# Kernel optimization log

Hardware: AMD Instinct MI355X
Metric: run time of the kernel (lower is better)

The kernel has to match this reference:

```python
import jax, jax.numpy as jnp
import numpy as np

B, KLEN, QLEN = 16, 4096, 1
D_MODEL, HEADS, KERNELS = 1024, 8, 10
DIM = D_MODEL // HEADS  # 128
SCALE = 0.02


def setup_inputs() -> dict:
    key = jax.random.key(0)
    ks = jax.random.split(key, 12)
    return {
        "query": jax.random.normal(ks[0], (B, QLEN, D_MODEL), jnp.float32),
        "key_in": jax.random.normal(ks[1], (B, KLEN, D_MODEL), jnp.float32),
        "value": jax.random.normal(ks[2], (B, KLEN, D_MODEL), jnp.float32),
        "prev_align": jax.random.uniform(ks[3], (B, HEADS, KLEN), jnp.float32),
        # learned params
        "conv_w": jax.random.normal(ks[4], (KERNELS, HEADS, 3), jnp.float32) * SCALE,   # OIH, k=3
        "conv_b": jnp.zeros((KERNELS,), jnp.float32),
        "w_u": jax.random.normal(ks[5], (KERNELS, DIM), jnp.float32) * SCALE,
        "w_q": jax.random.normal(ks[6], (D_MODEL, HEADS * DIM), jnp.float32) * SCALE,
        "w_v": jax.random.normal(ks[7], (D_MODEL, HEADS * DIM), jnp.float32) * SCALE,
        "bias": jax.random.uniform(ks[8], (DIM,), jnp.float32, minval=-0.1, maxval=0.1),
        "score_w": jax.random.normal(ks[9], (DIM,), jnp.float32) * SCALE,
        "score_b": jnp.zeros((), jnp.float32),
    }


def reference(query, key_in, value, prev_align, conv_w, conv_b, w_u, w_q, w_v, bias, score_w, score_b):
    b, k_len = key_in.shape[0], key_in.shape[1]
    # location features: conv1d over k_len with heads as channels -> [B, KERNELS, k_len]
    loc = jax.lax.conv_general_dilated(
        prev_align, conv_w, window_strides=(1,), padding=[(1, 1)],
        dimension_numbers=("NCH", "OIH", "NCH")) + conv_b[None, :, None]
    loc_energy = jnp.tanh(jnp.einsum("bck,cd->bkd", loc, w_u))  # [B, k_len, DIM]
    # projections split into heads
    q = jnp.einsum("bqf,fe->bqe", query, w_q).reshape(b, QLEN, HEADS, DIM).transpose(0, 2, 1, 3)   # [B,H,1,DIM]
    k = jnp.einsum("bkf,fe->bke", key_in, w_v).reshape(b, k_len, HEADS, DIM).transpose(0, 2, 1, 3)  # [B,H,K,DIM]
    v = value.reshape(b, k_len, HEADS, DIM).transpose(0, 2, 1, 3)                                   # [B,H,K,DIM]
    # additive energy (q_len==1 broadcasts over keys)
    e = jnp.tanh(k + q + loc_energy[:, None] + bias)            # [B,H,K,DIM]
    score = jnp.einsum("bhkd,d->bhk", e, score_w) + score_b    # [B,H,K]
    align = jax.nn.softmax(score, axis=-1)
    context = jnp.einsum("bhk,bhkd->bhd", align, v).reshape(b * HEADS, DIM)
    return context, align
```

## Files before the change

kernel.cpp:

```cpp
#include <hip/hip_runtime.h>
#include <hip/hip_bf16.h>
#include <cstdint>

typedef __attribute__((ext_vector_type(8))) short bf16x8;
typedef __attribute__((ext_vector_type(4))) float f32x4;
typedef __attribute__((ext_vector_type(8))) unsigned short u16x8;
typedef __attribute__((ext_vector_type(4))) unsigned int u32x4;

__device__ __forceinline__ unsigned short f2bf(float f) {
    unsigned int u = __float_as_uint(f);
    unsigned int r = (u + 0x7fffu + ((u >> 16) & 1u)) >> 16;
    return (unsigned short)r;
}

__device__ __forceinline__ float tanh_fast(float x) {
    return 1.0f - 2.0f / (__expf(2.0f * x) + 1.0f);
}

#define GLDS(SRC, DST) __builtin_amdgcn_global_load_lds(                         \
        (const __attribute__((address_space(1))) void*)(SRC),                    \
        (__attribute__((address_space(3))) void*)(DST), 16, 0, 0)

__global__ __launch_bounds__(256) void prep_kernel(
        const float* __restrict__ wv, unsigned short* __restrict__ wvT,
        const float* __restrict__ query, const float* __restrict__ w_q,
        float* __restrict__ ws_q,
        const float* __restrict__ pa, const float* __restrict__ conv_w,
        const float* __restrict__ conv_b, const float* __restrict__ w_u,
        float* __restrict__ le, float* __restrict__ ctx_out) {
    __shared__ __align__(16) char smem[16640];
    const int bid = blockIdx.x;
    const int t = threadIdx.x;

    if (bid < 256) {
        float (*tile)[129] = reinterpret_cast<float(*)[129]>(smem);
        const int h = bid >> 5, kt = bid & 31;
        for (int i = t; i < 1024; i += 256) {
            const int fl = i >> 5;
            const int e4 = (i & 31) * 4;
            const float4 v = *reinterpret_cast<const float4*>(
                wv + (size_t)(kt * 32 + fl) * 1024 + h * 128 + e4);
            tile[fl][e4 + 0] = v.x; tile[fl][e4 + 1] = v.y;
            tile[fl][e4 + 2] = v.z; tile[fl][e4 + 3] = v.w;
        }
        __syncthreads();
#pragma unroll
        for (int cc2 = 0; cc2 < 2; ++cc2) {
            const int c = cc2 * 256 + t;
            const int cb = c >> 6, kg = (c >> 4) & 3, ccl = c & 15;
            const int e_local = cb * 16 + ccl;
            u16x8 u;
#pragma unroll
            for (int jj = 0; jj < 8; ++jj) u[jj] = f2bf(tile[kg * 8 + jj][e_local]);
            *reinterpret_cast<u16x8*>(wvT + (((size_t)h * 32 + kt) * 512 + c) * 8) = u;
        }
    } else if (bid < 384) {
        float* qs = reinterpret_cast<float*>(smem);
        const int bh = bid - 256;
        const int b = bh >> 3, h = bh & 7;
        for (int i = t; i < 1024; i += 256) qs[i] = query[(size_t)b * 1024 + i];
        __syncthreads();
        if (t < 128) {
            float acc = 0.f;
            const float* wcol = w_q + h * 128 + t;
            for (int f = 0; f < 1024; ++f) acc = fmaf(qs[f], wcol[(size_t)f * 1024], acc);
            ws_q[(size_t)bh * 128 + t] = acc;
        }
    } else if (bid < 896) {
        float* pas = reinterpret_cast<float*>(smem);
        float* wu_s = pas + 1056;
        float* cw = wu_s + 1280;
        float* cb = cw + 240;
        const int idx = bid - 384;
        const int b = idx >> 5, k0 = (idx & 31) * 128;
        for (int i = t; i < 8 * 130; i += 256) {
            const int hh = i / 130, kk = i % 130;
            const int gk = k0 + kk - 1;
            pas[hh * 132 + kk] = (gk >= 0 && gk < 4096)
                ? pa[((size_t)(b * 8 + hh)) * 4096 + gk] : 0.f;
        }
        for (int i = t; i < 1280; i += 256) wu_s[i] = w_u[i];
        if (t < 240) cw[t] = conv_w[t];
        if (t < 10) cb[t] = conv_b[t];
        __syncthreads();
        const int k = t >> 1;
        const int d0 = (t & 1) * 64;
        float lc[10];
#pragma unroll
        for (int c = 0; c < 10; ++c) {
            float acc = cb[c];
#pragma unroll
            for (int hh = 0; hh < 8; ++hh) {
                acc += pas[hh * 132 + k] * cw[(c * 8 + hh) * 3 + 0]
                     + pas[hh * 132 + k + 1] * cw[(c * 8 + hh) * 3 + 1]
                     + pas[hh * 132 + k + 2] * cw[(c * 8 + hh) * 3 + 2];
            }
            lc[c] = acc;
        }
        float* dst = le + ((size_t)(b * 4096) + k0 + k) * 128 + d0;
#pragma unroll
        for (int dd = 0; dd < 64; dd += 4) {
            float4 o;
#pragma unroll
            for (int jj = 0; jj < 4; ++jj) {
                float s = 0.f;
#pragma unroll
                for (int c = 0; c < 10; ++c) s += lc[c] * wu_s[c * 128 + d0 + dd + jj];
                ((float*)&o)[jj] = tanh_fast(s);
            }
            *reinterpret_cast<float4*>(dst + dd) = o;
        }
    } else {
        float4 z = {0.f, 0.f, 0.f, 0.f};
        for (int i = t; i < 4096; i += 256)
            *reinterpret_cast<float4*>(ctx_out + (size_t)i * 4) = z;
    }
}

#define NT 32
__global__ __launch_bounds__(512) void gemm_score_kernel(
        const float* __restrict__ key_in, const unsigned short* __restrict__ wvT_tiled,
        const float* __restrict__ le,
        const float* __restrict__ ws_q, const float* __restrict__ bias,
        const float* __restrict__ score_w, const float* __restrict__ score_b,
        float* __restrict__ align_out) {
    __shared__ __align__(16) unsigned short As[3][4096];
    __shared__ __align__(16) unsigned short Bs[3][8192];
    __shared__ float qb_sm[256], sw_sm[128];
    __shared__ float partial[128][4];

    const int t = threadIdx.x;
    const int lane = t & 63, wid = t >> 6;
    const int wm = wid >> 2;
    const int wn = wid & 3;

    const int fid = blockIdx.x;
    const int x = fid & 7, j = fid >> 3;
    const int bm = x * 64 + (j >> 2);
    const int hp = j & 3;
    const int b = bm >> 5;
    const int kk0 = (bm & 31) << 7;

    if (t < 256) {
        const int hh = t >> 7, d = t & 127;
        qb_sm[t] = ws_q[(size_t)(b * 8 + hp * 2 + hh) * 128 + d] + bias[d];
        if (t < 128) sw_sm[t] = score_w[t];
    }

    const int r_ = t >> 2, ks = t & 3;
    const float* aRow = key_in + ((size_t)(b * 4096 + kk0) + r_) * 1024 + ks * 8;
    const int cW = (t >> 6) * 64 + ks * 16 + (r_ & 15);
    const int dst0 = (cW ^ (ks | ((ks & 1) << 2))) * 8;

    const int kgR = lane >> 4;
    const int laneSwz = lane ^ (kgR | ((kgR & 1) << 2));

    const unsigned short* bT = wvT_tiled
        + (size_t)(hp * 2 + (t >> 8)) * 131072 + (t & 255) * 8;
    const int dstB = (t >> 8) * 4096 + (t & 255) * 8;

    float4 st0, st1;

#define LOADA(KT) {                                                               \
        const float* p_ = aRow + (KT) * 32;                                       \
        st0 = *reinterpret_cast<const float4*>(p_);                               \
        st1 = *reinterpret_cast<const float4*>(p_ + 4); }

#define WRITEA(BUF) {                                                             \
        __hip_bfloat162 h0_ = __float22bfloat162_rn({st0.x, st0.y});              \
        __hip_bfloat162 h1_ = __float22bfloat162_rn({st0.z, st0.w});              \
        __hip_bfloat162 h2_ = __float22bfloat162_rn({st1.x, st1.y});              \
        __hip_bfloat162 h3_ = __float22bfloat162_rn({st1.z, st1.w});              \
        u32x4 u_;                                                                 \
        u_[0] = *reinterpret_cast<unsigned int*>(&h0_);                           \
        u_[1] = *reinterpret_cast<unsigned int*>(&h1_);                           \
        u_[2] = *reinterpret_cast<unsigned int*>(&h2_);                           \
        u_[3] = *reinterpret_cast<unsigned int*>(&h3_);                           \
        *reinterpret_cast<u32x4*>(&As[BUF][dst0]) = u_; }

#define STAGE_B(BUF, KT) {                                                        \
        GLDS(bT + (size_t)(KT) * 4096, &Bs[BUF][dstB]);                           \
        GLDS(bT + (size_t)(KT) * 4096 + 2048, &Bs[BUF][dstB + 2048]); }

    f32x4 acc[4][4] = {};

    LOADA(0);
    STAGE_B(0, 0);
    WRITEA(0);
    LOADA(1);

    for (int kt = 0; kt < NT; ++kt) {
        const int cur = kt % 3;
        const int nxt = (kt + 1) % 3;
        STAGE_B(nxt, (kt + 1) & (NT - 1));
        WRITEA(nxt);
        LOADA((kt + 2) & (NT - 1));
        asm volatile("s_waitcnt lgkmcnt(0)\n\t"
                     "s_barrier" ::: "memory");

        bf16x8 af[4], bg[4];
#pragma unroll
        for (int mf = 0; mf < 4; ++mf)
            af[mf] = *reinterpret_cast<const bf16x8*>(
                &As[cur][((wm * 4 + mf) * 64 + laneSwz) * 8]);
#pragma unroll
        for (int nf = 0; nf < 4; ++nf)
            bg[nf] = *reinterpret_cast<const bf16x8*>(
                &Bs[cur][(wn >> 1) * 4096 + ((wn & 1) * 4 + nf) * 512 + lane * 8]);
        __builtin_amdgcn_s_setprio(1);
#pragma unroll
        for (int mf = 0; mf < 4; ++mf)
#pragma unroll
            for (int nf = 0; nf < 4; ++nf)
                acc[mf][nf] = __builtin_amdgcn_mfma_f32_16x16x32_bf16(
                    af[mf], bg[nf], acc[mf][nf], 0, 0, 0);
        __builtin_amdgcn_s_setprio(0);
    }

    const float K2 = 2.8853900817779268f;
    const float sb = score_b[0];
    const int g = lane >> 4;
    const int l15 = lane & 15;
    float kqb[4], swv[4];
#pragma unroll
    for (int nf = 0; nf < 4; ++nf) {
        const int d128 = (wn & 1) * 64 + nf * 16 + l15;
        kqb[nf] = qb_sm[(wn >> 1) * 128 + d128] * K2;
        swv[nf] = sw_sm[d128];
    }
    const float* leB = le + ((size_t)(b * 4096 + kk0) + wm * 64 + g * 4) * 128
                       + (wn & 1) * 64 + l15;

#pragma unroll
    for (int mf = 0; mf < 4; ++mf) {
        float lv[16];
#pragma unroll
        for (int jj = 0; jj < 4; ++jj)
#pragma unroll
            for (int nf = 0; nf < 4; ++nf)
                lv[jj * 4 + nf] = leB[(size_t)(mf * 16 + jj) * 128 + nf * 16];
#pragma unroll
        for (int jj = 0; jj < 4; ++jj) {
            const int row_l = wm * 64 + mf * 16 + g * 4 + jj;
            float sum = 0.f;
#pragma unroll
            for (int nf = 0; nf < 4; ++nf) {
                const float m = fmaf(K2, lv[jj * 4 + nf], kqb[nf]);
                const float tt = fmaf(K2, acc[mf][nf][jj], m);
                const float y = __builtin_amdgcn_exp2f(tt);
                const float r = fmaf(-2.0f, __builtin_amdgcn_rcpf(y + 1.0f), 1.0f);
                sum = fmaf(r, swv[nf], sum);
            }
            sum += __shfl_xor(sum, 1);
            sum += __shfl_xor(sum, 2);
            sum += __shfl_xor(sum, 4);
            sum += __shfl_xor(sum, 8);
            if (l15 == 0) partial[row_l][wn] = sum;
        }
    }
    __syncthreads();
    if (t < 256) {
        const int r = t >> 1, hh = t & 1;
        const float sc = partial[r][hh * 2] + partial[r][hh * 2 + 1] + sb;
        align_out[(size_t)(b * 8 + hp * 2 + hh) * 4096 + kk0 + r] = sc;
    }
}

__global__ __launch_bounds__(256) void softmax_kernel(float* __restrict__ align_o) {
    const int bh = blockIdx.x;
    float* row = align_o + (size_t)bh * 4096;
    const int t = threadIdx.x;
    float v[16];
    float m = -1e30f;
#pragma unroll
    for (int i = 0; i < 16; ++i) {
        v[i] = row[i * 256 + t];
        m = fmaxf(m, v[i]);
    }
#pragma unroll
    for (int off = 32; off; off >>= 1) m = fmaxf(m, __shfl_xor(m, off));
    __shared__ float sm[4], ss[4];
    const int wid = t >> 6;
    if ((t & 63) == 0) sm[wid] = m;
    __syncthreads();
    m = fmaxf(fmaxf(sm[0], sm[1]), fmaxf(sm[2], sm[3]));
    float s = 0.f;
#pragma unroll
    for (int i = 0; i < 16; ++i) {
        v[i] = __expf(v[i] - m);
        s += v[i];
    }
#pragma unroll
    for (int off = 32; off; off >>= 1) s += __shfl_xor(s, off);
    if ((t & 63) == 0) ss[wid] = s;
    __syncthreads();
    s = ss[0] + ss[1] + ss[2] + ss[3];
    const float inv = 1.f / s;
#pragma unroll
    for (int i = 0; i < 16; ++i) row[i * 256 + t] = v[i] * inv;
}

__global__ __launch_bounds__(256) void ctx_partial_kernel(
        const float* __restrict__ value, const float* __restrict__ align_o,
        float* __restrict__ ctx_out) {
    const int s = blockIdx.x;
    const int bh = blockIdx.y;
    const int b = bh >> 3, h = bh & 7;
    const int t = threadIdx.x;
    const int d4 = (t & 31) * 4;
    const int kg = t >> 5;
    const float* arow = align_o + (size_t)bh * 4096 + s * 128;
    const float* vbase = value + ((size_t)(b * 4096 + s * 128)) * 1024 + h * 128 + d4;
    float4 acc = {0.f, 0.f, 0.f, 0.f};
    for (int i = 0; i < 16; ++i) {
        const int kk = i * 8 + kg;
        const float a = arow[kk];
        const float4 v = *reinterpret_cast<const float4*>(vbase + (size_t)kk * 1024);
        acc.x += a * v.x; acc.y += a * v.y; acc.z += a * v.z; acc.w += a * v.w;
    }
    __shared__ float sm2[8][128];
    *reinterpret_cast<float4*>(&sm2[kg][d4]) = acc;
    __syncthreads();
    if (t < 128) {
        float s0 = 0.f;
#pragma unroll
        for (int gg = 0; gg < 8; ++gg) s0 += sm2[gg][t];
        atomicAdd(&ctx_out[(size_t)bh * 128 + t], s0);
    }
}

extern "C" void kernel_launch(void* const* d_in, const int* in_sizes, int n_in,
                              void* d_out, int out_size, void* d_ws, size_t ws_size,
                              hipStream_t stream) {
    const float* query   = (const float*)d_in[0];
    const float* key_in  = (const float*)d_in[1];
    const float* value   = (const float*)d_in[2];
    const float* pa      = (const float*)d_in[3];
    const float* conv_w  = (const float*)d_in[4];
    const float* conv_b  = (const float*)d_in[5];
    const float* w_u     = (const float*)d_in[6];
    const float* w_q     = (const float*)d_in[7];
    const float* w_v     = (const float*)d_in[8];
    const float* bias    = (const float*)d_in[9];
    const float* score_w = (const float*)d_in[10];
    const float* score_b = (const float*)d_in[11];

    float* out = (float*)d_out;
    float* ctx_out = out;
    float* align_out = out + 16384;

    char* ws = (char*)d_ws;
    const size_t OFF_Q    = 0;
    const size_t OFF_WVT  = 65536;
    const size_t OFF_LE   = OFF_WVT + 2097152;

    float* ws_q            = (float*)(ws + OFF_Q);
    unsigned short* ws_wvT = (unsigned short*)(ws + OFF_WVT);
    float* ws_le           = (float*)(ws + OFF_LE);

    hipLaunchKernelGGL(prep_kernel, dim3(897), dim3(256), 0, stream,
                       w_v, ws_wvT, query, w_q, ws_q,
                       pa, conv_w, conv_b, w_u, ws_le, ctx_out);
    hipLaunchKernelGGL(gemm_score_kernel, dim3(2048), dim3(512), 0, stream,
                       key_in, ws_wvT, ws_le, ws_q, bias, score_w, score_b, align_out);
    hipLaunchKernelGGL(softmax_kernel, dim3(128), dim3(256), 0, stream, align_out);
    hipLaunchKernelGGL(ctx_partial_kernel, dim3(32, 128), dim3(256), 0, stream,
                       value, align_out, ctx_out);
}
```

Before: 286.9 us.

## Fuse softmax into score GEMM epilogue and context kernel via atomic row sums

Removes the separate softmax kernel. The score kernel now writes exp(score) without subtracting a row max and accumulates per-row sums with a shuffle reduction plus atomicAdd into a workspace buffer. The context kernel scales its partial sums and the stored align chunk by the reciprocal row sum. This saves one launch and a full read/write pass over the alignment matrix. In exchange it relies on scores being bounded (tanh times small weights) so that exp cannot overflow, and it adds atomics and a rowsum buffer that must be zeroed.

```diff
diff --git a/kernel.cpp b/kernel.cpp
--- a/kernel.cpp
+++ b/kernel.cpp
@@ -27,7 +27,8 @@
         float* __restrict__ ws_q,
         const float* __restrict__ pa, const float* __restrict__ conv_w,
         const float* __restrict__ conv_b, const float* __restrict__ w_u,
-        float* __restrict__ le, float* __restrict__ ctx_out) {
+        float* __restrict__ le, float* __restrict__ ctx_out,
+        float* __restrict__ rowsum) {
     __shared__ __align__(16) char smem[16640];
     const int bid = blockIdx.x;
     const int t = threadIdx.x;
@@ -114,6 +115,7 @@
         float4 z = {0.f, 0.f, 0.f, 0.f};
         for (int i = t; i < 4096; i += 256)
             *reinterpret_cast<float4*>(ctx_out + (size_t)i * 4) = z;
+        if (t < 128) rowsum[t] = 0.f;
     }
 }
 
@@ -123,7 +125,7 @@
         const float* __restrict__ le,
         const float* __restrict__ ws_q, const float* __restrict__ bias,
         const float* __restrict__ score_w, const float* __restrict__ score_b,
-        float* __restrict__ align_out) {
+        float* __restrict__ align_out, float* __restrict__ rowsum) {
     __shared__ __align__(16) unsigned short As[3][4096];
     __shared__ __align__(16) unsigned short Bs[3][8192];
     __shared__ float qb_sm[256], sw_sm[128];
@@ -218,6 +220,7 @@
     }
 
     const float K2 = 2.8853900817779268f;
+    const float LOG2E = 1.4426950408889634f;
     const float sb = score_b[0];
     const int g = lane >> 4;
     const int l15 = lane & 15;
@@ -262,54 +265,30 @@
     if (t < 256) {
         const int r = t >> 1, hh = t & 1;
         const float sc = partial[r][hh * 2] + partial[r][hh * 2 + 1] + sb;
-        align_out[(size_t)(b * 8 + hp * 2 + hh) * 4096 + kk0 + r] = sc;
-    }
-}
-
-__global__ __launch_bounds__(256) void softmax_kernel(float* __restrict__ align_o) {
-    const int bh = blockIdx.x;
-    float* row = align_o + (size_t)bh * 4096;
-    const int t = threadIdx.x;
-    float v[16];
-    float m = -1e30f;
-#pragma unroll
-    for (int i = 0; i < 16; ++i) {
-        v[i] = row[i * 256 + t];
-        m = fmaxf(m, v[i]);
-    }
-#pragma unroll
-    for (int off = 32; off; off >>= 1) m = fmaxf(m, __shfl_xor(m, off));
-    __shared__ float sm[4], ss[4];
-    const int wid = t >> 6;
-    if ((t & 63) == 0) sm[wid] = m;
-    __syncthreads();
-    m = fmaxf(fmaxf(sm[0], sm[1]), fmaxf(sm[2], sm[3]));
-    float s = 0.f;
-#pragma unroll
-    for (int i = 0; i < 16; ++i) {
-        v[i] = __expf(v[i] - m);
-        s += v[i];
-    }
-#pragma unroll
-    for (int off = 32; off; off >>= 1) s += __shfl_xor(s, off);
-    if ((t & 63) == 0) ss[wid] = s;
-    __syncthreads();
-    s = ss[0] + ss[1] + ss[2] + ss[3];
-    const float inv = 1.f / s;
-#pragma unroll
-    for (int i = 0; i < 16; ++i) row[i * 256 + t] = v[i] * inv;
+        const float e = __builtin_amdgcn_exp2f(sc * LOG2E);
+        align_out[(size_t)(b * 8 + hp * 2 + hh) * 4096 + kk0 + r] = e;
+        float s = e;
+        s += __shfl_xor(s, 2);
+        s += __shfl_xor(s, 4);
+        s += __shfl_xor(s, 8);
+        s += __shfl_xor(s, 16);
+        s += __shfl_xor(s, 32);
+        if ((lane >> 1) == 0)
+            atomicAdd(&rowsum[b * 8 + hp * 2 + hh], s);
+    }
 }
 
 __global__ __launch_bounds__(256) void ctx_partial_kernel(
-        const float* __restrict__ value, const float* __restrict__ align_o,
-        float* __restrict__ ctx_out) {
+        const float* __restrict__ value, float* __restrict__ align_o,
+        const float* __restrict__ rowsum, float* __restrict__ ctx_out) {
     const int s = blockIdx.x;
     const int bh = blockIdx.y;
     const int b = bh >> 3, h = bh & 7;
     const int t = threadIdx.x;
     const int d4 = (t & 31) * 4;
     const int kg = t >> 5;
-    const float* arow = align_o + (size_t)bh * 4096 + s * 128;
+    const float inv = 1.0f / rowsum[bh];
+    float* arow = align_o + (size_t)bh * 4096 + s * 128;
     const float* vbase = value + ((size_t)(b * 4096 + s * 128)) * 1024 + h * 128 + d4;
     float4 acc = {0.f, 0.f, 0.f, 0.f};
     for (int i = 0; i < 16; ++i) {
@@ -325,7 +304,8 @@
         float s0 = 0.f;
 #pragma unroll
         for (int gg = 0; gg < 8; ++gg) s0 += sm2[gg][t];
-        atomicAdd(&ctx_out[(size_t)bh * 128 + t], s0);
+        atomicAdd(&ctx_out[(size_t)bh * 128 + t], s0 * inv);
+        arow[t] *= inv;
     }
 }
 
@@ -351,19 +331,21 @@
 
     char* ws = (char*)d_ws;
     const size_t OFF_Q    = 0;
-    const size_t OFF_WVT  = 65536;
+    const size_t OFF_RS   = 65536;
+    const size_t OFF_WVT  = 66048;
     const size_t OFF_LE   = OFF_WVT + 2097152;
 
     float* ws_q            = (float*)(ws + OFF_Q);
+    float* ws_rs           = (float*)(ws + OFF_RS);
     unsigned short* ws_wvT = (unsigned short*)(ws + OFF_WVT);
     float* ws_le           = (float*)(ws + OFF_LE);
 
     hipLaunchKernelGGL(prep_kernel, dim3(897), dim3(256), 0, stream,
                        w_v, ws_wvT, query, w_q, ws_q,
-                       pa, conv_w, conv_b, w_u, ws_le, ctx_out);
+                       pa, conv_w, conv_b, w_u, ws_le, ctx_out, ws_rs);
     hipLaunchKernelGGL(gemm_score_kernel, dim3(2048), dim3(512), 0, stream,
-                       key_in, ws_wvT, ws_le, ws_q, bias, score_w, score_b, align_out);
-    hipLaunchKernelGGL(softmax_kernel, dim3(128), dim3(256), 0, stream, align_out);
+                       key_in, ws_wvT, ws_le, ws_q, bias, score_w, score_b,
+                       align_out, ws_rs);
     hipLaunchKernelGGL(ctx_partial_kernel, dim3(32, 128), dim3(256), 0, stream,
-                       value, align_out, ctx_out);
-}
+                       value, align_out, ws_rs, ctx_out);
+}
```

Result: no change. 285.7 us (-0.4%).
